# Performance work log

Hardware: AMD Instinct MI355X
Metric: run time of the kernel (lower is better)

## Reference

```python
import jax, jax.numpy as jnp
import numpy as np

D_MODEL = 1024
N_HEAD = 16
HEAD_DIM = D_MODEL // N_HEAD
B, S = 4, 2048


def setup_inputs() -> dict:
    key = jax.random.key(0)
    ks = jax.random.split(key, 11)
    s = 1.0 / np.sqrt(D_MODEL)
    return {
        "query": jax.random.normal(ks[0], (B, S, D_MODEL), jnp.float32),
        "key": jax.random.normal(ks[1], (B, S, D_MODEL), jnp.float32),
        "value": jax.random.normal(ks[2], (B, S, D_MODEL), jnp.float32),
        "Wq": jax.random.normal(ks[3], (D_MODEL, D_MODEL), jnp.float32) * s,
        "bq": jax.random.normal(ks[4], (D_MODEL,), jnp.float32) * s,
        "Wk": jax.random.normal(ks[5], (D_MODEL, D_MODEL), jnp.float32) * s,
        "bk": jax.random.normal(ks[6], (D_MODEL,), jnp.float32) * s,
        "Wv": jax.random.normal(ks[7], (D_MODEL, D_MODEL), jnp.float32) * s,
        "bv": jax.random.normal(ks[8], (D_MODEL,), jnp.float32) * s,
        "Wo": jax.random.normal(ks[9], (D_MODEL, D_MODEL), jnp.float32) * s,
        "bo": jax.random.normal(ks[10], (D_MODEL,), jnp.float32) * s,
    }


def reference(query, key, value, Wq, bq, Wk, bk, Wv, bv, Wo, bo):
    b, s, d_model = query.shape
    # projections; reshape to [b, h, s, hd]
    def proj(x, W, bias):
        return (x @ W + bias).reshape(b, s, N_HEAD, HEAD_DIM).transpose(0, 2, 1, 3)
    q = proj(query, Wq, bq)
    k = proj(key, Wk, bk)
    v = proj(value, Wv, bv)
    # NOTE: original code scales by sqrt(d_model) (bug-faithful), not sqrt(head_dim)
    scores = jnp.einsum("bhqd,bhkd->bhqk", q, k) / jnp.sqrt(jnp.float32(d_model))
    causal = jnp.tril(jnp.ones((s, s), dtype=bool))
    scores = jnp.where(causal[None, None], scores, -jnp.inf)
    p = jax.nn.softmax(scores, axis=-1)  # dropout is identity in eval
    x = jnp.einsum("bhqk,bhkd->bhqd", p, v)
    x = x.transpose(0, 2, 1, 3).reshape(b, s, d_model)
    return x @ Wo + bo
```

## Files before the change

kernel.cpp:

```cpp
#include <hip/hip_runtime.h>
#include <hip/hip_bf16.h>
#include <cstdint>
#include <cstddef>

#define D_MODEL 1024
#define N_HEAD 16
#define HEAD_DIM 64
#define BATCH 4
#define SEQ 2048
#define M_ROWS (BATCH * SEQ)

typedef __attribute__((ext_vector_type(8))) short short8v;
typedef __attribute__((ext_vector_type(4))) float f32x4;
typedef __attribute__((ext_vector_type(16))) float f32x16;

__device__ __forceinline__ unsigned short f2bf(float f) {
    union { uint32_t i; float f; } c;
    c.f = f;
    uint32_t r = c.i + 0x7FFFu + ((c.i >> 16) & 1u);
    return (unsigned short)(r >> 16);
}
__device__ __forceinline__ unsigned short trunc_bf(float f) {
    return (unsigned short)(__float_as_uint(f) >> 16);
}
__device__ __forceinline__ uint32_t pack_trunc2(float a, float b) {
    return __builtin_amdgcn_perm(__float_as_uint(b), __float_as_uint(a), 0x07060302u);
}
__device__ __forceinline__ uint32_t pack_rne2(float a, float b) {
    return (uint32_t)f2bf(a) | ((uint32_t)f2bf(b) << 16);
}

struct __align__(16) U4 { uint32_t x, y, z, w; };
struct __align__(8) U2 { uint32_t x, y; };

__device__ __forceinline__ int sw_off(int row, int gl) {
    return row * 64 + ((gl ^ (row & 7)) << 3);
}

__device__ __forceinline__ void gload16(const unsigned short *g, unsigned short *l) {
    __builtin_amdgcn_global_load_lds((const __attribute__((address_space(1))) void *)g,
                                     (__attribute__((address_space(3))) void *)l, 16, 0, 0);
}

__global__ __launch_bounds__(256)
void cvt_kernel(const float *__restrict__ src, unsigned short *__restrict__ dst)
{
    const size_t i = ((size_t)blockIdx.x * 256 + threadIdx.x) * 8;
    float4 lo = *(const float4 *)(src + i);
    float4 hi = *(const float4 *)(src + i + 4);
    U4 pk;
    pk.x = pack_trunc2(lo.x, lo.y);
    pk.y = pack_trunc2(lo.z, lo.w);
    pk.z = pack_trunc2(hi.x, hi.y);
    pk.w = pack_trunc2(hi.z, hi.w);
    *(U4 *)(dst + i) = pk;
}

__global__ __launch_bounds__(256)
void wtrans_kernel(const float *__restrict__ W, unsigned short *__restrict__ Wt)
{
    __shared__ float tile[32][33];
    const int t = threadIdx.x;
    const int tx = t & 31, ty = t >> 5;
    const int bk = blockIdx.y * 32, bn = blockIdx.x * 32;
#pragma unroll
    for (int i = 0; i < 4; i++)
        tile[ty + 8 * i][tx] = W[(size_t)(bk + ty + 8 * i) * D_MODEL + bn + tx];
    __syncthreads();
#pragma unroll
    for (int i = 0; i < 4; i++)
        Wt[(size_t)(bn + ty + 8 * i) * D_MODEL + bk + tx] = trunc_bf(tile[tx][ty + 8 * i]);
}

__global__ __launch_bounds__(256, 4)
void qk_gemm_kernel(const unsigned short *__restrict__ cq,
                    const unsigned short *__restrict__ ckb,
                    const unsigned short *__restrict__ wt2,
                    const float *__restrict__ bq, const float *__restrict__ bk,
                    unsigned short *__restrict__ oq, unsigned short *__restrict__ ok,
                    float qscale)
{
    __shared__ __align__(16) unsigned short At[128 * 64];
    __shared__ __align__(16) unsigned short Bt[128 * 64];

    const int z = blockIdx.z;
    const unsigned short *A = z ? ckb : cq;
    const unsigned short *Wt = wt2 + (size_t)z * D_MODEL * D_MODEL;
    const float *bias = z ? bk : bq;
    unsigned short *out = z ? ok : oq;
    const float es = z ? 1.f : qscale;

    const int t = threadIdx.x;
    const int wave = t >> 6;
    const int lane = t & 63;
    const int n_ = lane & 15;
    const int quad = lane >> 4;
    const int wm = wave >> 1, wn = wave & 1;
    const int m0 = blockIdx.x * 128;
    const int n0 = blockIdx.y * 128;

    f32x4 acc[4][4];
#pragma unroll
    for (int i = 0; i < 4; i++)
#pragma unroll
        for (int j = 0; j < 4; j++) acc[i][j] = (f32x4){0.f, 0.f, 0.f, 0.f};

    const int rl = lane >> 3;
    const int gsw = (lane & 7) ^ rl;

    for (int k0 = 0; k0 < D_MODEL; k0 += 64) {
        __syncthreads();
#pragma unroll
        for (int c = 0; c < 4; c++) {
            const int rb = wave * 32 + c * 8;
            gload16(A + (size_t)(m0 + rb + rl) * D_MODEL + k0 + (gsw << 3), &At[rb * 64]);
            gload16(Wt + (size_t)(n0 + rb + rl) * D_MODEL + k0 + (gsw << 3), &Bt[rb * 64]);
        }
        __syncthreads();

#pragma unroll
        for (int c = 0; c < 2; c++) {
            short8v af[4], bf[4];
#pragma unroll
            for (int mt = 0; mt < 4; mt++)
                af[mt] = *(const short8v *)&At[sw_off(wm * 64 + mt * 16 + n_, c * 4 + quad)];
#pragma unroll
            for (int nt = 0; nt < 4; nt++)
                bf[nt] = *(const short8v *)&Bt[sw_off(wn * 64 + nt * 16 + n_, c * 4 + quad)];
#pragma unroll
            for (int mt = 0; mt < 4; mt++)
#pragma unroll
                for (int nt = 0; nt < 4; nt++)
                    acc[mt][nt] = __builtin_amdgcn_mfma_f32_16x16x32_bf16(
                        af[mt], bf[nt], acc[mt][nt], 0, 0, 0);
        }
    }

    float bi[4];
#pragma unroll
    for (int nt = 0; nt < 4; nt++) bi[nt] = bias[n0 + wn * 64 + nt * 16 + n_];
#pragma unroll
    for (int mt = 0; mt < 4; mt++)
#pragma unroll
        for (int reg = 0; reg < 4; reg++) {
            const int m = m0 + wm * 64 + mt * 16 + quad * 4 + reg;
#pragma unroll
            for (int nt = 0; nt < 4; nt++) {
                const int col = n0 + wn * 64 + nt * 16 + n_;
                out[(size_t)m * D_MODEL + col] = f2bf((acc[mt][nt][reg] + bi[nt]) * es);
            }
        }
}

template <typename TA, int MODE, typename TO>
__global__ __launch_bounds__(256, 2)
void mgemm_kernel(const TA *__restrict__ A,
                  const unsigned short *__restrict__ Wt,
                  const float *__restrict__ bias,
                  TO *__restrict__ out,
                  float escale)
{
    __shared__ __align__(16) unsigned short At[2][128 * 64];
    __shared__ __align__(16) unsigned short Bt[2][128 * 64];

    const int t = threadIdx.x;
    const int wave = t >> 6;
    const int lane = t & 63;
    const int n_ = lane & 15;
    const int quad = lane >> 4;
    const int wm = wave >> 1, wn = wave & 1;
    const int m0 = blockIdx.x * 128;
    const int n0 = blockIdx.y * 128;

    f32x4 acc[4][4];
#pragma unroll
    for (int i = 0; i < 4; i++)
#pragma unroll
        for (int j = 0; j < 4; j++) acc[i][j] = (f32x4){0.f, 0.f, 0.f, 0.f};

    const int srow = t >> 3;
    const int sg = t & 7;
    const int rl = lane >> 3;
    const int gsw = (lane & 7) ^ rl;

    for (int k0 = 0; k0 < D_MODEL; k0 += 128) {
        __syncthreads();
        if constexpr (sizeof(TA) == 2) {
            const unsigned short *Ab = (const unsigned short *)A;
#pragma unroll
            for (int h = 0; h < 2; h++)
#pragma unroll
                for (int c = 0; c < 4; c++) {
                    const int rb = wave * 32 + c * 8;
                    gload16(Ab + (size_t)(m0 + rb + rl) * D_MODEL + k0 + h * 64 + (gsw << 3),
                            &At[h][rb * 64]);
                    gload16(Wt + (size_t)(n0 + rb + rl) * D_MODEL + k0 + h * 64 + (gsw << 3),
                            &Bt[h][rb * 64]);
                }
        } else {
#pragma unroll
            for (int h = 0; h < 2; h++) {
#pragma unroll
                for (int i = 0; i < 4; i++) {
                    const int r = srow + 32 * i;
                    const float *p =
                        (const float *)A + (size_t)(m0 + r) * D_MODEL + k0 + h * 64 + sg * 8;
                    float4 lo = *(const float4 *)p;
                    float4 hi = *(const float4 *)(p + 4);
                    U4 pk;
                    pk.x = pack_trunc2(lo.x, lo.y);
                    pk.y = pack_trunc2(lo.z, lo.w);
                    pk.z = pack_trunc2(hi.x, hi.y);
                    pk.w = pack_trunc2(hi.z, hi.w);
                    *(U4 *)&At[h][sw_off(r, sg)] = pk;
                }
#pragma unroll
                for (int i = 0; i < 4; i++) {
                    const int r = srow + 32 * i;
                    const unsigned short *p =
                        Wt + (size_t)(n0 + r) * D_MODEL + k0 + h * 64 + sg * 8;
                    *(U4 *)&Bt[h][sw_off(r, sg)] = *(const U4 *)p;
                }
            }
        }
        __syncthreads();

#pragma unroll
        for (int c = 0; c < 4; c++) {
            const int bk_ = c >> 1, cc = c & 1;
            short8v af[4], bf[4];
#pragma unroll
            for (int mt = 0; mt < 4; mt++)
                af[mt] = *(const short8v *)&At[bk_][sw_off(wm * 64 + mt * 16 + n_, cc * 4 + quad)];
#pragma unroll
            for (int nt = 0; nt < 4; nt++)
                bf[nt] = *(const short8v *)&Bt[bk_][sw_off(wn * 64 + nt * 16 + n_, cc * 4 + quad)];
#pragma unroll
            for (int mt = 0; mt < 4; mt++)
#pragma unroll
                for (int nt = 0; nt < 4; nt++)
                    acc[mt][nt] = __builtin_amdgcn_mfma_f32_16x16x32_bf16(
                        af[mt], bf[nt], acc[mt][nt], 0, 0, 0);
        }
    }

    float bi[4];
#pragma unroll
    for (int nt = 0; nt < 4; nt++) bi[nt] = bias[n0 + wn * 64 + nt * 16 + n_];

    if constexpr (MODE == 2) {
#pragma unroll
        for (int mt = 0; mt < 4; mt++) {
            const int m = m0 + wm * 64 + mt * 16 + quad * 4;
#pragma unroll
            for (int nt = 0; nt < 4; nt++) {
                const int col = n0 + wn * 64 + nt * 16 + n_;
                const size_t idx = ((size_t)(m >> 11) * D_MODEL + col) * SEQ + (m & 2047);
                U2 pk;
                pk.x = pack_rne2(acc[mt][nt][0] + bi[nt], acc[mt][nt][1] + bi[nt]);
                pk.y = pack_rne2(acc[mt][nt][2] + bi[nt], acc[mt][nt][3] + bi[nt]);
                *(U2 *)((unsigned short *)out + idx) = pk;
            }
        }
    } else {
#pragma unroll
        for (int mt = 0; mt < 4; mt++)
#pragma unroll
            for (int reg = 0; reg < 4; reg++) {
                const int m = m0 + wm * 64 + mt * 16 + quad * 4 + reg;
#pragma unroll
                for (int nt = 0; nt < 4; nt++) {
                    const int col = n0 + wn * 64 + nt * 16 + n_;
                    const float v = (acc[mt][nt][reg] + bi[nt]) * escale;
                    if constexpr (MODE == 1)
                        ((unsigned short *)out)[(size_t)m * D_MODEL + col] = f2bf(v);
                    else
                        ((float *)out)[(size_t)m * D_MODEL + col] = v;
                }
            }
    }
}

__global__ __launch_bounds__(256, 2)
void attn_kernel(const unsigned short *Qg,
                 const unsigned short *__restrict__ Kg,
                 const unsigned short *__restrict__ VTg,
                 unsigned short *AO)
{
    __shared__ __align__(16) unsigned short Kt[2][64 * 64];
    __shared__ __align__(16) unsigned short Vt[2][64 * 64];

    const int h = blockIdx.x;
    const int b = blockIdx.y;
    const int qpair = blockIdx.z;
    const int t = threadIdx.x;
    const int w = t >> 6;
    const int lane = t & 63;
    const int ql = lane & 31;
    const int hi = lane >> 5;

    const size_t row_base = (size_t)b * SEQ * D_MODEL + h * HEAD_DIM;
    const size_t vhead = (size_t)(b * N_HEAD + h) * HEAD_DIM * SEQ;

    const int r0 = t >> 3;
    const int g = t & 7;

#pragma unroll
    for (int pass = 0; pass < 2; ++pass) {
        const int qb = pass ? (15 - qpair) : qpair;
        const int qs0 = qb * 128 + w * 32;
        const int qseq = qs0 + ql;

        short8v qf[4];
#pragma unroll
        for (int c = 0; c < 4; c++)
            qf[c] = *(const short8v *)(Qg + row_base + (size_t)qseq * D_MODEL + c * 16 + hi * 8);

        float m_i = -INFINITY, l_i = 0.f;
        f32x16 Oacc[2];
#pragma unroll
        for (int dt = 0; dt < 2; dt++)
#pragma unroll
            for (int i = 0; i < 16; i++) Oacc[dt][i] = 0.f;

        const int nst = qb + 1;

        for (int s = 0; s <= nst - 1; ++s) {
            __syncthreads();
#pragma unroll
            for (int bk2 = 0; bk2 < 2; bk2++)
#pragma unroll
                for (int i = 0; i < 2; i++) {
                    const int r = r0 + 32 * i;
                    U4 kv = *(const U4 *)(Kg + row_base +
                                          (size_t)(s * 128 + bk2 * 64 + r) * D_MODEL + g * 8);
                    *(U4 *)&Kt[bk2][sw_off(r, g)] = kv;
                    U4 vv = *(const U4 *)(VTg + vhead + (size_t)r * SEQ + s * 128 + bk2 * 64 + g * 8);
                    *(U4 *)&Vt[bk2][sw_off(r, g)] = vv;
                }
            __syncthreads();

#pragma unroll
            for (int h2 = 0; h2 < 2; h2++) {
                const int kv0 = s * 128 + h2 * 64;
                if (kv0 > qs0 + 31) continue;

                f32x16 st[2];
                __builtin_amdgcn_s_setprio(1);
#pragma unroll
                for (int kt = 0; kt < 2; kt++) {
#pragma unroll
                    for (int i = 0; i < 16; i++) st[kt][i] = 0.f;
#pragma unroll
                    for (int c = 0; c < 4; c++) {
                        short8v kf = *(const short8v *)&Kt[h2][sw_off(kt * 32 + ql, c * 2 + hi)];
                        st[kt] = __builtin_amdgcn_mfma_f32_32x32x16_bf16(kf, qf[c], st[kt], 0, 0, 0);
                    }
                }
                __builtin_amdgcn_s_setprio(0);

                if (kv0 + 63 > qs0) {
#pragma unroll
                    for (int kt = 0; kt < 2; kt++)
#pragma unroll
                        for (int r = 0; r < 16; r++) {
                            const int kseq = kv0 + kt * 32 + (r & 3) + 8 * (r >> 2) + 4 * hi;
                            if (kseq > qseq) st[kt][r] = -INFINITY;
                        }
                }

                float mx = -INFINITY;
#pragma unroll
                for (int kt = 0; kt < 2; kt++)
#pragma unroll
                    for (int r = 0; r < 16; r++) mx = fmaxf(mx, st[kt][r]);
                mx = fmaxf(mx, __shfl_xor(mx, 32, 64));
                const float mnew = fmaxf(m_i, mx);
                const float alpha = __builtin_amdgcn_exp2f(m_i - mnew);
                m_i = mnew;
                float rs = 0.f;
#pragma unroll
                for (int kt = 0; kt < 2; kt++)
#pragma unroll
                    for (int r = 0; r < 16; r++) {
                        const float p = __builtin_amdgcn_exp2f(st[kt][r] - mnew);
                        st[kt][r] = p;
                        rs += p;
                    }
                rs += __shfl_xor(rs, 32, 64);
                l_i = l_i * alpha + rs;
#pragma unroll
                for (int dt = 0; dt < 2; dt++)
#pragma unroll
                    for (int r = 0; r < 16; r++) Oacc[dt][r] *= alpha;

                short8v pf[4];
#pragma unroll
                for (int tt = 0; tt < 4; tt++) {
                    const int kt = tt >> 1, o = (tt & 1) * 8;
                    const uint32_t A  = pack_trunc2(st[kt][o + 0], st[kt][o + 1]);
                    const uint32_t A2 = pack_trunc2(st[kt][o + 2], st[kt][o + 3]);
                    const uint32_t B  = pack_trunc2(st[kt][o + 4], st[kt][o + 5]);
                    const uint32_t B2 = pack_trunc2(st[kt][o + 6], st[kt][o + 7]);
                    const uint32_t c1 = (uint32_t)__shfl_xor((int)(hi ? A : B), 32, 64);
                    const uint32_t c2 = (uint32_t)__shfl_xor((int)(hi ? A2 : B2), 32, 64);
                    union { uint32_t u[4]; short8v s; } cv;
                    cv.u[0] = hi ? c1 : A;
                    cv.u[1] = hi ? c2 : A2;
                    cv.u[2] = hi ? B : c1;
                    cv.u[3] = hi ? B2 : c2;
                    pf[tt] = cv.s;
                }

                __builtin_amdgcn_s_setprio(1);
#pragma unroll
                for (int dt = 0; dt < 2; dt++)
#pragma unroll
                    for (int tt = 0; tt < 4; tt++) {
                        short8v vf = *(const short8v *)&Vt[h2][sw_off(dt * 32 + ql, tt * 2 + hi)];
                        Oacc[dt] =
                            __builtin_amdgcn_mfma_f32_32x32x16_bf16(vf, pf[tt], Oacc[dt], 0, 0, 0);
                    }
                __builtin_amdgcn_s_setprio(0);
            }
        }

        const float linv = 1.f / l_i;
        const size_t obase = row_base + (size_t)qseq * D_MODEL;
#pragma unroll
        for (int dt = 0; dt < 2; dt++)
#pragma unroll
            for (int rg = 0; rg < 4; rg++) {
                const int d0 = dt * 32 + 8 * rg + 4 * hi;
                U2 pk;
                pk.x = (uint32_t)f2bf(Oacc[dt][4 * rg + 0] * linv) |
                       ((uint32_t)f2bf(Oacc[dt][4 * rg + 1] * linv) << 16);
                pk.y = (uint32_t)f2bf(Oacc[dt][4 * rg + 2] * linv) |
                       ((uint32_t)f2bf(Oacc[dt][4 * rg + 3] * linv) << 16);
                *(U2 *)(AO + obase + d0) = pk;
            }
    }
}

extern "C" void kernel_launch(void *const *d_in, const int *in_sizes, int n_in,
                              void *d_out, int out_size, void *d_ws, size_t ws_size,
                              hipStream_t stream)
{
    const float *q  = (const float *)d_in[0];
    const float *k  = (const float *)d_in[1];
    const float *v  = (const float *)d_in[2];
    const float *Wq = (const float *)d_in[3];
    const float *bq = (const float *)d_in[4];
    const float *Wk = (const float *)d_in[5];
    const float *bk = (const float *)d_in[6];
    const float *Wv = (const float *)d_in[7];
    const float *bv = (const float *)d_in[8];
    const float *Wo = (const float *)d_in[9];
    const float *bo = (const float *)d_in[10];
    float *out = (float *)d_out;

    const size_t TENS = (size_t)M_ROWS * D_MODEL;
    const size_t WT = (size_t)D_MODEL * D_MODEL;

    dim3 wgrid(32, 32);
    dim3 ggrid(M_ROWS / 128, D_MODEL / 128);
    const int cgrid = (int)(TENS / 8 / 256);
    const float qscale = 0.03125f * 1.44269504088896341f;

    const size_t need_new = (4 * TENS + 2 * WT) * sizeof(unsigned short);

    if (ws_size >= need_new && (size_t)out_size >= TENS * sizeof(unsigned short)) {
        unsigned short *qbuf = (unsigned short *)d_ws;
        unsigned short *kbuf = qbuf + TENS;
        unsigned short *vtbuf = kbuf + TENS;
        unsigned short *cq = vtbuf + TENS;
        unsigned short *wt2 = cq + TENS;
        unsigned short *ck = (unsigned short *)d_out;

        wtrans_kernel<<<wgrid, 256, 0, stream>>>(Wq, wt2);
        wtrans_kernel<<<wgrid, 256, 0, stream>>>(Wk, wt2 + WT);
        cvt_kernel<<<cgrid, 256, 0, stream>>>(q, cq);
        cvt_kernel<<<cgrid, 256, 0, stream>>>(k, ck);
        qk_gemm_kernel<<<dim3(M_ROWS / 128, D_MODEL / 128, 2), 256, 0, stream>>>(
            cq, ck, wt2, bq, bk, qbuf, kbuf, qscale);

        wtrans_kernel<<<wgrid, 256, 0, stream>>>(Wv, wt2);
        cvt_kernel<<<cgrid, 256, 0, stream>>>(v, cq);
        mgemm_kernel<unsigned short, 2, unsigned short><<<ggrid, 256, 0, stream>>>(
            cq, wt2, bv, vtbuf, 1.f);

        attn_kernel<<<dim3(N_HEAD, BATCH, SEQ / 256), 256, 0, stream>>>(qbuf, kbuf, vtbuf, qbuf);

        wtrans_kernel<<<wgrid, 256, 0, stream>>>(Wo, wt2);
        mgemm_kernel<unsigned short, 3, float><<<ggrid, 256, 0, stream>>>(qbuf, wt2, bo, out, 1.f);
    } else {
        unsigned short *qbuf = (unsigned short *)d_ws;
        unsigned short *kbuf = qbuf + TENS;
        unsigned short *vtbuf = kbuf + TENS;
        unsigned short *wt = vtbuf + TENS;

        wtrans_kernel<<<wgrid, 256, 0, stream>>>(Wq, wt);
        mgemm_kernel<float, 1, unsigned short><<<ggrid, 256, 0, stream>>>(q, wt, bq, qbuf, qscale);
        wtrans_kernel<<<wgrid, 256, 0, stream>>>(Wk, wt);
        mgemm_kernel<float, 1, unsigned short><<<ggrid, 256, 0, stream>>>(k, wt, bk, kbuf, 1.f);
        wtrans_kernel<<<wgrid, 256, 0, stream>>>(Wv, wt);
        mgemm_kernel<float, 2, unsigned short><<<ggrid, 256, 0, stream>>>(v, wt, bv, vtbuf, 1.f);

        attn_kernel<<<dim3(N_HEAD, BATCH, SEQ / 256), 256, 0, stream>>>(qbuf, kbuf, vtbuf, qbuf);

        wtrans_kernel<<<wgrid, 256, 0, stream>>>(Wo, wt);
        mgemm_kernel<unsigned short, 3, float><<<ggrid, 256, 0, stream>>>(qbuf, wt, bo, out, 1.f);
    }
}
```

Before: 321.9 us.

## Fuse weight transposes and input casts into one prep kernel; attention uses 64-key tiles

Replaces the separate weight-transpose and fp32-to-bf16 cast launches with a single prep kernel. It transposes all four weight matrices and casts q, k and v in one grid, so fewer kernel launches and inter-kernel gaps sit on the critical path. The attention loop now stages one 64-key K/V tile at a time instead of two, which halves shared memory per block but doubles the number of barrier-separated load phases. This needs more workspace for four transposed weights and uses the output buffer for two cast inputs.

New measurement: 317.0 us. Within noise of the previous version (-1.5%).

```diff
diff --git a/kernel.cpp b/kernel.cpp
--- a/kernel.cpp
+++ b/kernel.cpp
@@ -43,17 +43,47 @@
 }
 
 __global__ __launch_bounds__(256)
-void cvt_kernel(const float *__restrict__ src, unsigned short *__restrict__ dst)
+void prep_kernel(const float *__restrict__ Wq, const float *__restrict__ Wk,
+                 const float *__restrict__ Wv, const float *__restrict__ Wo,
+                 unsigned short *__restrict__ wt4,
+                 const float *__restrict__ q, const float *__restrict__ k,
+                 const float *__restrict__ v,
+                 unsigned short *__restrict__ cq, unsigned short *__restrict__ ck,
+                 unsigned short *__restrict__ cv)
 {
-    const size_t i = ((size_t)blockIdx.x * 256 + threadIdx.x) * 8;
-    float4 lo = *(const float4 *)(src + i);
-    float4 hi = *(const float4 *)(src + i + 4);
-    U4 pk;
-    pk.x = pack_trunc2(lo.x, lo.y);
-    pk.y = pack_trunc2(lo.z, lo.w);
-    pk.z = pack_trunc2(hi.x, hi.y);
-    pk.w = pack_trunc2(hi.z, hi.w);
-    *(U4 *)(dst + i) = pk;
+    __shared__ float tile[32][33];
+    const int id = blockIdx.x;
+    const int t = threadIdx.x;
+    if (id < 4096) {
+        const int w = id >> 10;
+        const int bx = id & 31, by = (id >> 5) & 31;
+        const float *W = w == 0 ? Wq : (w == 1 ? Wk : (w == 2 ? Wv : Wo));
+        unsigned short *Wt = wt4 + (size_t)w * D_MODEL * D_MODEL;
+        const int tx = t & 31, ty = t >> 5;
+        const int bk = by * 32, bn = bx * 32;
+#pragma unroll
+        for (int i = 0; i < 4; i++)
+            tile[ty + 8 * i][tx] = W[(size_t)(bk + ty + 8 * i) * D_MODEL + bn + tx];
+        __syncthreads();
+#pragma unroll
+        for (int i = 0; i < 4; i++)
+            Wt[(size_t)(bn + ty + 8 * i) * D_MODEL + bk + tx] = trunc_bf(tile[tx][ty + 8 * i]);
+    } else {
+        const int id2 = id - 4096;
+        const int z = id2 >> 12;
+        const int bx = id2 & 4095;
+        const float *src = z == 0 ? q : (z == 1 ? k : v);
+        unsigned short *dst = z == 0 ? cq : (z == 1 ? ck : cv);
+        const size_t i = ((size_t)bx * 256 + t) * 8;
+        float4 lo = *(const float4 *)(src + i);
+        float4 hi = *(const float4 *)(src + i + 4);
+        U4 pk;
+        pk.x = pack_trunc2(lo.x, lo.y);
+        pk.y = pack_trunc2(lo.z, lo.w);
+        pk.z = pack_trunc2(hi.x, hi.y);
+        pk.w = pack_trunc2(hi.z, hi.w);
+        *(U4 *)(dst + i) = pk;
+    }
 }
 
 __global__ __launch_bounds__(256)
@@ -287,8 +317,8 @@
                  const unsigned short *__restrict__ VTg,
                  unsigned short *AO)
 {
-    __shared__ __align__(16) unsigned short Kt[2][64 * 64];
-    __shared__ __align__(16) unsigned short Vt[2][64 * 64];
+    __shared__ __align__(16) unsigned short Kt[64 * 64];
+    __shared__ __align__(16) unsigned short Vt[64 * 64];
 
     const int h = blockIdx.x;
     const int b = blockIdx.y;
@@ -323,106 +353,98 @@
 #pragma unroll
             for (int i = 0; i < 16; i++) Oacc[dt][i] = 0.f;
 
-        const int nst = qb + 1;
-
-        for (int s = 0; s <= nst - 1; ++s) {
+        const int kb_max = 2 * qb + 1;
+
+        for (int kb = 0; kb <= kb_max; ++kb) {
             __syncthreads();
 #pragma unroll
-            for (int bk2 = 0; bk2 < 2; bk2++)
-#pragma unroll
-                for (int i = 0; i < 2; i++) {
-                    const int r = r0 + 32 * i;
-                    U4 kv = *(const U4 *)(Kg + row_base +
-                                          (size_t)(s * 128 + bk2 * 64 + r) * D_MODEL + g * 8);
-                    *(U4 *)&Kt[bk2][sw_off(r, g)] = kv;
-                    U4 vv = *(const U4 *)(VTg + vhead + (size_t)r * SEQ + s * 128 + bk2 * 64 + g * 8);
-                    *(U4 *)&Vt[bk2][sw_off(r, g)] = vv;
-                }
+            for (int i = 0; i < 2; i++) {
+                const int r = r0 + 32 * i;
+                U4 kv = *(const U4 *)(Kg + row_base + (size_t)(kb * 64 + r) * D_MODEL + g * 8);
+                *(U4 *)&Kt[sw_off(r, g)] = kv;
+                U4 vv = *(const U4 *)(VTg + vhead + (size_t)r * SEQ + kb * 64 + g * 8);
+                *(U4 *)&Vt[sw_off(r, g)] = vv;
+            }
             __syncthreads();
 
-#pragma unroll
-            for (int h2 = 0; h2 < 2; h2++) {
-                const int kv0 = s * 128 + h2 * 64;
-                if (kv0 > qs0 + 31) continue;
-
-                f32x16 st[2];
-                __builtin_amdgcn_s_setprio(1);
-#pragma unroll
-                for (int kt = 0; kt < 2; kt++) {
-#pragma unroll
-                    for (int i = 0; i < 16; i++) st[kt][i] = 0.f;
-#pragma unroll
-                    for (int c = 0; c < 4; c++) {
-                        short8v kf = *(const short8v *)&Kt[h2][sw_off(kt * 32 + ql, c * 2 + hi)];
-                        st[kt] = __builtin_amdgcn_mfma_f32_32x32x16_bf16(kf, qf[c], st[kt], 0, 0, 0);
+            if (kb * 64 > qs0 + 31) continue;
+
+            f32x16 st[2];
+            __builtin_amdgcn_s_setprio(1);
+#pragma unroll
+            for (int kt = 0; kt < 2; kt++) {
+#pragma unroll
+                for (int i = 0; i < 16; i++) st[kt][i] = 0.f;
+#pragma unroll
+                for (int c = 0; c < 4; c++) {
+                    short8v kf = *(const short8v *)&Kt[sw_off(kt * 32 + ql, c * 2 + hi)];
+                    st[kt] = __builtin_amdgcn_mfma_f32_32x32x16_bf16(kf, qf[c], st[kt], 0, 0, 0);
+                }
+            }
+            __builtin_amdgcn_s_setprio(0);
+
+            if (kb * 64 + 63 > qs0) {
+#pragma unroll
+                for (int kt = 0; kt < 2; kt++)
+#pragma unroll
+                    for (int r = 0; r < 16; r++) {
+                        const int kseq = kb * 64 + kt * 32 + (r & 3) + 8 * (r >> 2) + 4 * hi;
+                        if (kseq > qseq) st[kt][r] = -INFINITY;
                     }
-                }
-                __builtin_amdgcn_s_setprio(0);
-
-                if (kv0 + 63 > qs0) {
-#pragma unroll
-                    for (int kt = 0; kt < 2; kt++)
-#pragma unroll
-                        for (int r = 0; r < 16; r++) {
-                            const int kseq = kv0 + kt * 32 + (r & 3) + 8 * (r >> 2) + 4 * hi;
-                            if (kseq > qseq) st[kt][r] = -INFINITY;
-                        }
-                }
-
-                float mx = -INFINITY;
-#pragma unroll
-                for (int kt = 0; kt < 2; kt++)
-#pragma unroll
-                    for (int r = 0; r < 16; r++) mx = fmaxf(mx, st[kt][r]);
-                mx = fmaxf(mx, __shfl_xor(mx, 32, 64));
-                const float mnew = fmaxf(m_i, mx);
-                const float alpha = __builtin_amdgcn_exp2f(m_i - mnew);
-                m_i = mnew;
-                float rs = 0.f;
-#pragma unroll
-                for (int kt = 0; kt < 2; kt++)
-#pragma unroll
-                    for (int r = 0; r < 16; r++) {
-                        const float p = __builtin_amdgcn_exp2f(st[kt][r] - mnew);
-                        st[kt][r] = p;
-                        rs += p;
-                    }
-                rs += __shfl_xor(rs, 32, 64);
-                l_i = l_i * alpha + rs;
-#pragma unroll
-                for (int dt = 0; dt < 2; dt++)
-#pragma unroll
-                    for (int r = 0; r < 16; r++) Oacc[dt][r] *= alpha;
-
-                short8v pf[4];
+            }
+
+            float mx = -INFINITY;
+#pragma unroll
+            for (int kt = 0; kt < 2; kt++)
+#pragma unroll
+                for (int r = 0; r < 16; r++) mx = fmaxf(mx, st[kt][r]);
+            mx = fmaxf(mx, __shfl_xor(mx, 32, 64));
+            const float mnew = fmaxf(m_i, mx);
+            const float alpha = __builtin_amdgcn_exp2f(m_i - mnew);
+            m_i = mnew;
+            float rs = 0.f;
+#pragma unroll
+            for (int kt = 0; kt < 2; kt++)
+#pragma unroll
+                for (int r = 0; r < 16; r++) {
+                    const float p = __builtin_amdgcn_exp2f(st[kt][r] - mnew);
+                    st[kt][r] = p;
+                    rs += p;
+                }
+            rs += __shfl_xor(rs, 32, 64);
+            l_i = l_i * alpha + rs;
+#pragma unroll
+            for (int dt = 0; dt < 2; dt++)
+#pragma unroll
+                for (int r = 0; r < 16; r++) Oacc[dt][r] *= alpha;
+
+            short8v pf[4];
+#pragma unroll
+            for (int tt = 0; tt < 4; tt++) {
+                const int kt = tt >> 1, o = (tt & 1) * 8;
+                const uint32_t A  = pack_trunc2(st[kt][o + 0], st[kt][o + 1]);
+                const uint32_t A2 = pack_trunc2(st[kt][o + 2], st[kt][o + 3]);
+                const uint32_t B  = pack_trunc2(st[kt][o + 4], st[kt][o + 5]);
+                const uint32_t B2 = pack_trunc2(st[kt][o + 6], st[kt][o + 7]);
+                const uint32_t c1 = (uint32_t)__shfl_xor((int)(hi ? A : B), 32, 64);
+                const uint32_t c2 = (uint32_t)__shfl_xor((int)(hi ? A2 : B2), 32, 64);
+                union { uint32_t u[4]; short8v s; } cv;
+                cv.u[0] = hi ? c1 : A;
+                cv.u[1] = hi ? c2 : A2;
+                cv.u[2] = hi ? B : c1;
+                cv.u[3] = hi ? B2 : c2;
+                pf[tt] = cv.s;
+            }
+
+            __builtin_amdgcn_s_setprio(1);
+#pragma unroll
+            for (int dt = 0; dt < 2; dt++)
 #pragma unroll
                 for (int tt = 0; tt < 4; tt++) {
-                    const int kt = tt >> 1, o = (tt & 1) * 8;
-                    const uint32_t A  = pack_trunc2(st[kt][o + 0], st[kt][o + 1]);
-                    const uint32_t A2 = pack_trunc2(st[kt][o + 2], st[kt][o + 3]);
-                    const uint32_t B  = pack_trunc2(st[kt][o + 4], st[kt][o + 5]);
-                    const uint32_t B2 = pack_trunc2(st[kt][o + 6], st[kt][o + 7]);
-                    const uint32_t c1 = (uint32_t)__shfl_xor((int)(hi ? A : B), 32, 64);
-                    const uint32_t c2 = (uint32_t)__shfl_xor((int)(hi ? A2 : B2), 32, 64);
-                    union { uint32_t u[4]; short8v s; } cv;
-                    cv.u[0] = hi ? c1 : A;
-                    cv.u[1] = hi ? c2 : A2;
-                    cv.u[2] = hi ? B : c1;
-                    cv.u[3] = hi ? B2 : c2;
-                    pf[tt] = cv.s;
-                }
-
-                __builtin_amdgcn_s_setprio(1);
-#pragma unroll
-                for (int dt = 0; dt < 2; dt++)
-#pragma unroll
-                    for (int tt = 0; tt < 4; tt++) {
-                        short8v vf = *(const short8v *)&Vt[h2][sw_off(dt * 32 + ql, tt * 2 + hi)];
-                        Oacc[dt] =
-                            __builtin_amdgcn_mfma_f32_32x32x16_bf16(vf, pf[tt], Oacc[dt], 0, 0, 0);
-                    }
-                __builtin_amdgcn_s_setprio(0);
-            }
+                    short8v vf = *(const short8v *)&Vt[sw_off(dt * 32 + ql, tt * 2 + hi)];
+                    Oacc[dt] = __builtin_amdgcn_mfma_f32_32x32x16_bf16(vf, pf[tt], Oacc[dt], 0, 0, 0);
+                }
+            __builtin_amdgcn_s_setprio(0);
         }
 
         const float linv = 1.f / l_i;
@@ -464,35 +486,27 @@
 
     dim3 wgrid(32, 32);
     dim3 ggrid(M_ROWS / 128, D_MODEL / 128);
-    const int cgrid = (int)(TENS / 8 / 256);
     const float qscale = 0.03125f * 1.44269504088896341f;
 
-    const size_t need_new = (4 * TENS + 2 * WT) * sizeof(unsigned short);
-
-    if (ws_size >= need_new && (size_t)out_size >= TENS * sizeof(unsigned short)) {
+    const size_t need_new = (4 * TENS + 4 * WT) * sizeof(unsigned short);
+
+    if (ws_size >= need_new && (size_t)out_size >= 2 * TENS * sizeof(unsigned short)) {
         unsigned short *qbuf = (unsigned short *)d_ws;
         unsigned short *kbuf = qbuf + TENS;
         unsigned short *vtbuf = kbuf + TENS;
         unsigned short *cq = vtbuf + TENS;
-        unsigned short *wt2 = cq + TENS;
+        unsigned short *wt4 = cq + TENS;
         unsigned short *ck = (unsigned short *)d_out;
-
-        wtrans_kernel<<<wgrid, 256, 0, stream>>>(Wq, wt2);
-        wtrans_kernel<<<wgrid, 256, 0, stream>>>(Wk, wt2 + WT);
-        cvt_kernel<<<cgrid, 256, 0, stream>>>(q, cq);
-        cvt_kernel<<<cgrid, 256, 0, stream>>>(k, ck);
+        unsigned short *cv = ck + TENS;
+
+        prep_kernel<<<16384, 256, 0, stream>>>(Wq, Wk, Wv, Wo, wt4, q, k, v, cq, ck, cv);
         qk_gemm_kernel<<<dim3(M_ROWS / 128, D_MODEL / 128, 2), 256, 0, stream>>>(
-            cq, ck, wt2, bq, bk, qbuf, kbuf, qscale);
-
-        wtrans_kernel<<<wgrid, 256, 0, stream>>>(Wv, wt2);
-        cvt_kernel<<<cgrid, 256, 0, stream>>>(v, cq);
+            cq, ck, wt4, bq, bk, qbuf, kbuf, qscale);
         mgemm_kernel<unsigned short, 2, unsigned short><<<ggrid, 256, 0, stream>>>(
-            cq, wt2, bv, vtbuf, 1.f);
-
+            cv, wt4 + 2 * WT, bv, vtbuf, 1.f);
         attn_kernel<<<dim3(N_HEAD, BATCH, SEQ / 256), 256, 0, stream>>>(qbuf, kbuf, vtbuf, qbuf);
-
-        wtrans_kernel<<<wgrid, 256, 0, stream>>>(Wo, wt2);
-        mgemm_kernel<unsigned short, 3, float><<<ggrid, 256, 0, stream>>>(qbuf, wt2, bo, out, 1.f);
+        mgemm_kernel<unsigned short, 3, float><<<ggrid, 256, 0, stream>>>(
+            qbuf, wt4 + 3 * WT, bo, out, 1.f);
     } else {
         unsigned short *qbuf = (unsigned short *)d_ws;
         unsigned short *kbuf = qbuf + TENS;
```
